# Performance work log

Hardware: AMD Instinct MI355X
Metric: run time of the kernel (lower is better)

## Reference

```python
import jax, jax.numpy as jnp
import numpy as np


def setup_inputs() -> dict:
    key = jax.random.key(0)
    k1, k2 = jax.random.split(key)
    context_emb = jax.random.normal(k1, (8, 2048, 768), dtype=jnp.float32)
    query_emb = jax.random.normal(k2, (8, 512, 768), dtype=jnp.float32)
    return {"context_emb": context_emb, "query_emb": query_emb}


def reference(context_emb, query_emb):
    # temp[b, q, c] = sum_d query[b,q,d] * context[b,c,d]
    temp = jnp.einsum("bqd,bcd->bqc", query_emb, context_emb)
    # softmax over the query axis (dim=1 in torch)
    alpha = jax.nn.softmax(temp, axis=1)  # [B, Lq, Lc]
    # attention_weighted_query[b, c, d] = sum_q query[b,q,d] * alpha[b,q,c]
    awq = jnp.einsum("bqd,bqc->bcd", query_emb, alpha)  # [B, Lc, D]
    # elementwise gate against context
    return context_emb * awq
```

## Files before the change

### kernel.cpp

```cpp
#include <hip/hip_runtime.h>

#define NB 8
#define LQ 512
#define LC 2048
#define DD 768

typedef _Float16 f16x8 __attribute__((ext_vector_type(8)));
typedef _Float16 f16x4 __attribute__((ext_vector_type(4)));
typedef float    f32x4 __attribute__((ext_vector_type(4)));

__global__ __launch_bounds__(256) void preconvert_q(const float* __restrict__ Q,
                                                    _Float16* __restrict__ Qh,
                                                    _Float16* __restrict__ QhT) {
    __shared__ _Float16 lt[64][68];
    const int blk = blockIdx.x;
    const int b   = blk / 96;
    const int rem = blk % 96;
    const int q0  = (rem / 12) * 64;
    const int d0  = (rem % 12) * 64;
    const int t   = threadIdx.x;
    const int tr  = t >> 4;
    const int tc  = t & 15;

    const float* Qb  = Q  + ((size_t)b * LQ + q0) * DD + d0;
    _Float16*    Qhb = Qh + ((size_t)b * LQ + q0) * DD + d0;

#pragma unroll
    for (int i = 0; i < 4; i++) {
        const int row = i * 16 + tr;
        const int col = tc * 4;
        f32x4 v = *(const f32x4*)(Qb + (size_t)row * DD + col);
        f16x4 h;
        h.x = (_Float16)v.x; h.y = (_Float16)v.y;
        h.z = (_Float16)v.z; h.w = (_Float16)v.w;
        *(f16x4*)(Qhb + (size_t)row * DD + col) = h;
        *(f16x4*)&lt[row][col] = h;
    }
    __syncthreads();

    _Float16* QTb = QhT + ((size_t)b * DD + d0) * LQ + q0;
#pragma unroll
    for (int i = 0; i < 4; i++) {
        const int drow = i * 16 + tr;
        const int qc   = tc * 4;
        f16x4 h;
        h.x = lt[qc + 0][drow];
        h.y = lt[qc + 1][drow];
        h.z = lt[qc + 2][drow];
        h.w = lt[qc + 3][drow];
        *(f16x4*)(QTb + (size_t)drow * LQ + qc) = h;
    }
}

#define CM        64
#define A_SLOTS   96
#define P_OFF     98304
#define P_SLOTS   64
#define SMEM_BYTES 163840

__global__ __launch_bounds__(512, 2) void gated_attn(const float* __restrict__ ctx,
                                                     const _Float16* __restrict__ Qh,
                                                     const _Float16* __restrict__ QhT,
                                                     float* __restrict__ out) {
    __shared__ __align__(16) char smem[SMEM_BYTES];
    float (*red_max)[64] = (float (*)[64])(smem + P_OFF);
    float (*red_sum)[64] = (float (*)[64])(smem + P_OFF + 2048);

    const int b    = blockIdx.x & 7;
    const int c0   = (blockIdx.x >> 3) * CM;
    const int t    = threadIdx.x;
    const int w    = t >> 6;
    const int lane = t & 63;
    const int quad = lane >> 4;
    const int l15  = lane & 15;

    const float*    Cb  = ctx + ((size_t)b * LC + c0) * DD;
    const _Float16* Qhb = Qh  + (size_t)b * LQ * DD;
    const _Float16* QTb = QhT + (size_t)b * DD * LQ;

    const _Float16* bqb = Qhb + (size_t)(w * 64 + l15) * DD + quad * 8;
    const _Float16* cqb = QTb + (size_t)(w * 96 + l15) * LQ + quad * 8;

#pragma unroll
    for (int i = 0; i < 12; i++) {
        const int idx = i * 512 + t;
        const int row = idx / 96;
        const int c16 = idx % 96;
        const float* p = Cb + (size_t)row * DD + c16 * 8;
        f32x4 f0 = *(const f32x4*)p;
        f32x4 f1 = *(const f32x4*)(p + 4);
        f16x8 v;
        v[0] = (_Float16)f0.x; v[1] = (_Float16)f0.y;
        v[2] = (_Float16)f0.z; v[3] = (_Float16)f0.w;
        v[4] = (_Float16)f1.x; v[5] = (_Float16)f1.y;
        v[6] = (_Float16)f1.z; v[7] = (_Float16)f1.w;
        const int s16 = row * A_SLOTS + ((c16 & ~7) | ((c16 ^ row) & 7));
        *(f16x8*)(smem + (size_t)s16 * 16) = v;
    }
    f16x8 bq0[4];
#pragma unroll
    for (int nt = 0; nt < 4; nt++)
        bq0[nt] = *(const f16x8*)(bqb + (size_t)(nt * 16) * DD);
    __syncthreads();

    f32x4 acc[4][4];
#pragma unroll
    for (int mt = 0; mt < 4; mt++)
#pragma unroll
        for (int nt = 0; nt < 4; nt++)
            acc[mt][nt] = (f32x4){0.f, 0.f, 0.f, 0.f};

#pragma unroll
    for (int kc = 0; kc < 24; kc++) {
        const int c16 = kc * 4 + quad;
        const int sw  = (c16 & ~7) | ((c16 ^ l15) & 7);
        f16x8 a[4];
#pragma unroll
        for (int mt = 0; mt < 4; mt++)
            a[mt] = *(const f16x8*)(smem + (size_t)((mt * 16 + l15) * A_SLOTS + sw) * 16);
        f16x8 bq[4];
#pragma unroll
        for (int nt = 0; nt < 4; nt++)
            bq[nt] = (kc == 0) ? bq0[nt]
                   : *(const f16x8*)(bqb + (size_t)(nt * 16) * DD + kc * 32);
#pragma unroll
        for (int nt = 0; nt < 4; nt++)
#pragma unroll
            for (int mt = 0; mt < 4; mt++)
                acc[mt][nt] = __builtin_amdgcn_mfma_f32_16x16x32_f16(a[mt], bq[nt], acc[mt][nt], 0, 0, 0);
    }

    f16x8 cq0[6];
#pragma unroll
    for (int nt = 0; nt < 6; nt++)
        cq0[nt] = *(const f16x8*)(cqb + (size_t)(nt * 16) * LQ);

    float rm[4][4];
#pragma unroll
    for (int mt = 0; mt < 4; mt++)
#pragma unroll
        for (int r = 0; r < 4; r++)
            rm[mt][r] = -1e30f;
#pragma unroll
    for (int mt = 0; mt < 4; mt++)
#pragma unroll
        for (int nt = 0; nt < 4; nt++) {
            rm[mt][0] = fmaxf(rm[mt][0], acc[mt][nt].x);
            rm[mt][1] = fmaxf(rm[mt][1], acc[mt][nt].y);
            rm[mt][2] = fmaxf(rm[mt][2], acc[mt][nt].z);
            rm[mt][3] = fmaxf(rm[mt][3], acc[mt][nt].w);
        }
#pragma unroll
    for (int off = 1; off < 16; off <<= 1)
#pragma unroll
        for (int mt = 0; mt < 4; mt++)
#pragma unroll
            for (int r = 0; r < 4; r++)
                rm[mt][r] = fmaxf(rm[mt][r], __shfl_xor(rm[mt][r], off));
    if (l15 == 0) {
#pragma unroll
        for (int mt = 0; mt < 4; mt++)
#pragma unroll
            for (int r = 0; r < 4; r++)
                red_max[w][mt * 16 + quad * 4 + r] = rm[mt][r];
    }
    __syncthreads();

    float fm[4][4];
#pragma unroll
    for (int mt = 0; mt < 4; mt++)
#pragma unroll
        for (int r = 0; r < 4; r++) {
            const int row = mt * 16 + quad * 4 + r;
            float m0 = fmaxf(fmaxf(red_max[0][row], red_max[1][row]),
                             fmaxf(red_max[2][row], red_max[3][row]));
            float m1 = fmaxf(fmaxf(red_max[4][row], red_max[5][row]),
                             fmaxf(red_max[6][row], red_max[7][row]));
            fm[mt][r] = fmaxf(m0, m1);
        }
    float rs[4][4];
#pragma unroll
    for (int mt = 0; mt < 4; mt++)
#pragma unroll
        for (int r = 0; r < 4; r++)
            rs[mt][r] = 0.f;
#pragma unroll
    for (int mt = 0; mt < 4; mt++)
#pragma unroll
        for (int nt = 0; nt < 4; nt++) {
            float e0 = __expf(acc[mt][nt].x - fm[mt][0]);
            float e1 = __expf(acc[mt][nt].y - fm[mt][1]);
            float e2 = __expf(acc[mt][nt].z - fm[mt][2]);
            float e3 = __expf(acc[mt][nt].w - fm[mt][3]);
            acc[mt][nt].x = e0; acc[mt][nt].y = e1;
            acc[mt][nt].z = e2; acc[mt][nt].w = e3;
            rs[mt][0] += e0; rs[mt][1] += e1; rs[mt][2] += e2; rs[mt][3] += e3;
        }
#pragma unroll
    for (int off = 1; off < 16; off <<= 1)
#pragma unroll
        for (int mt = 0; mt < 4; mt++)
#pragma unroll
            for (int r = 0; r < 4; r++)
                rs[mt][r] += __shfl_xor(rs[mt][r], off);
    if (l15 == 0) {
#pragma unroll
        for (int mt = 0; mt < 4; mt++)
#pragma unroll
            for (int r = 0; r < 4; r++)
                red_sum[w][mt * 16 + quad * 4 + r] = rs[mt][r];
    }
    __syncthreads();

#pragma unroll
    for (int mt = 0; mt < 4; mt++)
#pragma unroll
        for (int r = 0; r < 4; r++) {
            const int row = mt * 16 + quad * 4 + r;
            float s = 0.f;
#pragma unroll
            for (int j = 0; j < 8; j++) s += red_sum[j][row];
            const float inv = 1.0f / s;
#pragma unroll
            for (int nt = 0; nt < 4; nt++) {
                acc[mt][nt].x = (r == 0) ? acc[mt][nt].x * inv : acc[mt][nt].x;
                acc[mt][nt].y = (r == 1) ? acc[mt][nt].y * inv : acc[mt][nt].y;
                acc[mt][nt].z = (r == 2) ? acc[mt][nt].z * inv : acc[mt][nt].z;
                acc[mt][nt].w = (r == 3) ? acc[mt][nt].w * inv : acc[mt][nt].w;
            }
        }
    __syncthreads();

#pragma unroll
    for (int mt = 0; mt < 4; mt++)
#pragma unroll
        for (int r = 0; r < 4; r++) {
            const int row = mt * 16 + quad * 4 + r;
#pragma unroll
            for (int nt = 0; nt < 4; nt++) {
                const int q = w * 64 + nt * 16 + l15;
                float v = (r == 0 ? acc[mt][nt].x : r == 1 ? acc[mt][nt].y
                          : r == 2 ? acc[mt][nt].z : acc[mt][nt].w);
                const int c16 = q >> 3;
                const int s16 = row * P_SLOTS + ((c16 & ~7) | ((c16 ^ row) & 7));
                *(_Float16*)(smem + P_OFF + (size_t)s16 * 16 + (q & 7) * 2) = (_Float16)v;
            }
        }
    __syncthreads();

    f32x4 acc2[4][6];
#pragma unroll
    for (int mt = 0; mt < 4; mt++)
#pragma unroll
        for (int nt = 0; nt < 6; nt++)
            acc2[mt][nt] = (f32x4){0.f, 0.f, 0.f, 0.f};

#pragma unroll
    for (int kc = 0; kc < 16; kc++) {
        const int c16 = kc * 4 + quad;
        const int sw  = (c16 & ~7) | ((c16 ^ l15) & 7);
        f16x8 pf[4];
#pragma unroll
        for (int mt = 0; mt < 4; mt++)
            pf[mt] = *(const f16x8*)(smem + P_OFF + (size_t)((mt * 16 + l15) * P_SLOTS + sw) * 16);
        f16x8 cq[6];
#pragma unroll
        for (int nt = 0; nt < 6; nt++)
            cq[nt] = (kc == 0) ? cq0[nt]
                   : *(const f16x8*)(cqb + (size_t)(nt * 16) * LQ + kc * 32);
#pragma unroll
        for (int nt = 0; nt < 6; nt++)
#pragma unroll
            for (int mt = 0; mt < 4; mt++)
                acc2[mt][nt] = __builtin_amdgcn_mfma_f32_16x16x32_f16(pf[mt], cq[nt], acc2[mt][nt], 0, 0, 0);
    }

#pragma unroll
    for (int mt = 0; mt < 4; mt++)
#pragma unroll
        for (int nt = 0; nt < 6; nt++) {
            const int col = w * 96 + nt * 16 + l15;
            const int c16 = col >> 3;
            const int sub = col & 7;
#pragma unroll
            for (int r = 0; r < 4; r++) {
                const int rl  = mt * 16 + quad * 4 + r;
                const int s16 = rl * A_SLOTS + ((c16 & ~7) | ((c16 ^ rl) & 7));
                const float g = (float)*(const _Float16*)(smem + (size_t)s16 * 16 + sub * 2);
                float v = (r == 0 ? acc2[mt][nt].x : r == 1 ? acc2[mt][nt].y
                          : r == 2 ? acc2[mt][nt].z : acc2[mt][nt].w);
                out[((size_t)b * LC + c0 + rl) * DD + col] = g * v;
            }
        }
}

extern "C" void kernel_launch(void* const* d_in, const int* in_sizes, int n_in,
                              void* d_out, int out_size, void* d_ws, size_t ws_size,
                              hipStream_t stream) {
    const float* ctx = (const float*)d_in[0];
    const float* q   = (const float*)d_in[1];
    float* out = (float*)d_out;

    const size_t nQ = (size_t)NB * LQ * DD;
    _Float16* Qh  = (_Float16*)d_ws;
    _Float16* QhT = Qh + nQ;

    preconvert_q<<<dim3(NB * 96), dim3(256), 0, stream>>>(q, Qh, QhT);
    gated_attn<<<dim3(NB * (LC / CM)), dim3(512), 0, stream>>>(ctx, Qh, QhT, out);
}
```

Before: 154.8 us.

## Stage Q operands in LDS via async global_load_lds double buffering

Both GEMM phases now read their Q operand from LDS instead of global memory. Each chunk is loaded with direct global-to-LDS DMA into a double buffer and prefetched one k-step ahead, with an XOR swizzle to avoid bank conflicts and s_setprio raised around the MFMA bursts. The LDS layout is reorganised so the probability tile overwrites the context tile region, which means the final gate now re-reads the fp32 context from global memory. This adds a block-wide barrier every k-step and extra global reads of the context in the epilogue.

```diff
diff --git a/kernel.cpp b/kernel.cpp
--- a/kernel.cpp
+++ b/kernel.cpp
@@ -54,17 +54,26 @@
 
 #define CM        64
 #define A_SLOTS   96
-#define P_OFF     98304
 #define P_SLOTS   64
+#define RED_OFF   65536
+#define BBUF_OFF  98304
+#define CBUF_OFF  65536
 #define SMEM_BYTES 163840
+
+__device__ __forceinline__ void dma16(const _Float16* g, char* l) {
+    __builtin_amdgcn_global_load_lds(
+        (const __attribute__((address_space(1))) unsigned int*)g,
+        (__attribute__((address_space(3))) unsigned int*)l,
+        16, 0, 0);
+}
 
 __global__ __launch_bounds__(512, 2) void gated_attn(const float* __restrict__ ctx,
                                                      const _Float16* __restrict__ Qh,
                                                      const _Float16* __restrict__ QhT,
                                                      float* __restrict__ out) {
     __shared__ __align__(16) char smem[SMEM_BYTES];
-    float (*red_max)[64] = (float (*)[64])(smem + P_OFF);
-    float (*red_sum)[64] = (float (*)[64])(smem + P_OFF + 2048);
+    float (*red_max)[64] = (float (*)[64])(smem + RED_OFF);
+    float (*red_sum)[64] = (float (*)[64])(smem + RED_OFF + 2048);
 
     const int b    = blockIdx.x & 7;
     const int c0   = (blockIdx.x >> 3) * CM;
@@ -78,8 +87,17 @@
     const _Float16* Qhb = Qh  + (size_t)b * LQ * DD;
     const _Float16* QTb = QhT + (size_t)b * DD * LQ;
 
-    const _Float16* bqb = Qhb + (size_t)(w * 64 + l15) * DD + quad * 8;
-    const _Float16* cqb = QTb + (size_t)(w * 96 + l15) * LQ + quad * 8;
+    const int srow = t >> 2;
+    const int sse  = (t & 3) ^ (srow & 3) ^ ((srow >> 2) & 3);
+    const _Float16* stA = Qhb + (size_t)srow * DD + sse * 8;
+    const _Float16* stC = QTb + (size_t)srow * LQ + sse * 8;
+    char* ldsW = smem + (size_t)w * 1024;
+
+    const int bsub = ((quad ^ (l15 & 3) ^ ((l15 >> 2) & 3)) & 3) * 16;
+
+#pragma unroll
+    for (int j = 0; j < 4; j++)
+        dma16(stA + (size_t)(j * 128) * DD, ldsW + BBUF_OFF + j * 8192);
 
 #pragma unroll
     for (int i = 0; i < 12; i++) {
@@ -97,10 +115,6 @@
         const int s16 = row * A_SLOTS + ((c16 & ~7) | ((c16 ^ row) & 7));
         *(f16x8*)(smem + (size_t)s16 * 16) = v;
     }
-    f16x8 bq0[4];
-#pragma unroll
-    for (int nt = 0; nt < 4; nt++)
-        bq0[nt] = *(const f16x8*)(bqb + (size_t)(nt * 16) * DD);
     __syncthreads();
 
     f32x4 acc[4][4];
@@ -112,28 +126,32 @@
 
 #pragma unroll
     for (int kc = 0; kc < 24; kc++) {
+        if (kc > 0) __syncthreads();
+        if (kc + 1 < 24) {
+            char* nb = ldsW + BBUF_OFF + ((kc + 1) & 1) * 32768;
+            const _Float16* src = stA + (kc + 1) * 32;
+#pragma unroll
+            for (int j = 0; j < 4; j++)
+                dma16(src + (size_t)(j * 128) * DD, nb + j * 8192);
+        }
+        const char* bbuf = smem + BBUF_OFF + (kc & 1) * 32768;
         const int c16 = kc * 4 + quad;
         const int sw  = (c16 & ~7) | ((c16 ^ l15) & 7);
-        f16x8 a[4];
+        f16x8 a[4], bq[4];
 #pragma unroll
         for (int mt = 0; mt < 4; mt++)
             a[mt] = *(const f16x8*)(smem + (size_t)((mt * 16 + l15) * A_SLOTS + sw) * 16);
-        f16x8 bq[4];
 #pragma unroll
         for (int nt = 0; nt < 4; nt++)
-            bq[nt] = (kc == 0) ? bq0[nt]
-                   : *(const f16x8*)(bqb + (size_t)(nt * 16) * DD + kc * 32);
+            bq[nt] = *(const f16x8*)(bbuf + (size_t)(w * 64 + nt * 16 + l15) * 64 + bsub);
+        __builtin_amdgcn_s_setprio(1);
 #pragma unroll
         for (int nt = 0; nt < 4; nt++)
 #pragma unroll
             for (int mt = 0; mt < 4; mt++)
                 acc[mt][nt] = __builtin_amdgcn_mfma_f32_16x16x32_f16(a[mt], bq[nt], acc[mt][nt], 0, 0, 0);
-    }
-
-    f16x8 cq0[6];
-#pragma unroll
-    for (int nt = 0; nt < 6; nt++)
-        cq0[nt] = *(const f16x8*)(cqb + (size_t)(nt * 16) * LQ);
+        __builtin_amdgcn_s_setprio(0);
+    }
 
     float rm[4][4];
 #pragma unroll
@@ -232,6 +250,10 @@
     __syncthreads();
 
 #pragma unroll
+    for (int j = 0; j < 6; j++)
+        dma16(stC + (size_t)(j * 128) * LQ, ldsW + CBUF_OFF + j * 8192);
+
+#pragma unroll
     for (int mt = 0; mt < 4; mt++)
 #pragma unroll
         for (int r = 0; r < 4; r++) {
@@ -243,7 +265,7 @@
                           : r == 2 ? acc[mt][nt].z : acc[mt][nt].w);
                 const int c16 = q >> 3;
                 const int s16 = row * P_SLOTS + ((c16 & ~7) | ((c16 ^ row) & 7));
-                *(_Float16*)(smem + P_OFF + (size_t)s16 * 16 + (q & 7) * 2) = (_Float16)v;
+                *(_Float16*)(smem + (size_t)s16 * 16 + (q & 7) * 2) = (_Float16)v;
             }
         }
     __syncthreads();
@@ -257,22 +279,31 @@
 
 #pragma unroll
     for (int kc = 0; kc < 16; kc++) {
+        if (kc > 0) __syncthreads();
+        if (kc + 1 < 16) {
+            char* nb = ldsW + CBUF_OFF + ((kc + 1) & 1) * 49152;
+            const _Float16* src = stC + (kc + 1) * 32;
+#pragma unroll
+            for (int j = 0; j < 6; j++)
+                dma16(src + (size_t)(j * 128) * LQ, nb + j * 8192);
+        }
+        const char* cbuf = smem + CBUF_OFF + (kc & 1) * 49152;
         const int c16 = kc * 4 + quad;
         const int sw  = (c16 & ~7) | ((c16 ^ l15) & 7);
-        f16x8 pf[4];
-#pragma unroll
-        for (int mt = 0; mt < 4; mt++)
-            pf[mt] = *(const f16x8*)(smem + P_OFF + (size_t)((mt * 16 + l15) * P_SLOTS + sw) * 16);
-        f16x8 cq[6];
+        f16x8 pf[4], cq[6];
+#pragma unroll
+        for (int mt = 0; mt < 4; mt++)
+            pf[mt] = *(const f16x8*)(smem + (size_t)((mt * 16 + l15) * P_SLOTS + sw) * 16);
 #pragma unroll
         for (int nt = 0; nt < 6; nt++)
-            cq[nt] = (kc == 0) ? cq0[nt]
-                   : *(const f16x8*)(cqb + (size_t)(nt * 16) * LQ + kc * 32);
+            cq[nt] = *(const f16x8*)(cbuf + (size_t)(w * 96 + nt * 16 + l15) * 64 + bsub);
+        __builtin_amdgcn_s_setprio(1);
 #pragma unroll
         for (int nt = 0; nt < 6; nt++)
 #pragma unroll
             for (int mt = 0; mt < 4; mt++)
                 acc2[mt][nt] = __builtin_amdgcn_mfma_f32_16x16x32_f16(pf[mt], cq[nt], acc2[mt][nt], 0, 0, 0);
+        __builtin_amdgcn_s_setprio(0);
     }
 
 #pragma unroll
@@ -280,16 +311,13 @@
 #pragma unroll
         for (int nt = 0; nt < 6; nt++) {
             const int col = w * 96 + nt * 16 + l15;
-            const int c16 = col >> 3;
-            const int sub = col & 7;
 #pragma unroll
             for (int r = 0; r < 4; r++) {
                 const int rl  = mt * 16 + quad * 4 + r;
-                const int s16 = rl * A_SLOTS + ((c16 & ~7) | ((c16 ^ rl) & 7));
-                const float g = (float)*(const _Float16*)(smem + (size_t)s16 * 16 + sub * 2);
+                const size_t idx = ((size_t)b * LC + c0 + rl) * DD + col;
                 float v = (r == 0 ? acc2[mt][nt].x : r == 1 ? acc2[mt][nt].y
                           : r == 2 ? acc2[mt][nt].z : acc2[mt][nt].w);
-                out[((size_t)b * LC + c0 + rl) * DD + col] = g * v;
+                out[idx] = ctx[idx] * v;
             }
         }
 }
```

Result: no change. 151.8 us (-1.9%).
